# Kernel tuning notes

Hardware: AMD Instinct MI355X
Metric: run time of the kernel (lower is better)

The kernel has to match this reference:

```python
import jax, jax.numpy as jnp
import numpy as np

EPS = 1e-6
H, KV, HD, FF = 16, 8, 128, 3072

def rmsnorm(x, scale):
    # qwen3_compatible: compute in fp32, scale, cast back
    xf = x.astype(jnp.float32)
    var = jnp.mean(xf * xf, axis=-1, keepdims=True)
    return ((xf * jax.lax.rsqrt(var + EPS)) * scale).astype(x.dtype)

def apply_rope(x, cos, sin):
    # x: [b, h, s, d]; cos/sin: [s, d]
    d = x.shape[-1]
    x1, x2 = x[..., : d // 2], x[..., d // 2 :]
    rotated = jnp.concatenate([-x2, x1], axis=-1)
    return (x * cos[None, None] + rotated * sin[None, None]).astype(x.dtype)

def setup_inputs() -> dict:
    key = jax.random.key(0)
    B, S, D = 2, 2048, 1024
    ks = jax.random.split(key, 8)
    x = jax.random.normal(ks[0], (B, S, D), jnp.float32)
    mask = jnp.triu(jnp.ones((S, S), dtype=bool), k=1)  # True = masked (causal)
    # Qwen3 RoPE, base 1e6, full-dim cos/sin (halves duplicated)
    pos = jnp.arange(S, dtype=jnp.float32)
    inv_freq = 1.0 / (1e6 ** (jnp.arange(0, HD, 2, dtype=jnp.float32) / HD))
    ang = pos[:, None] * inv_freq[None, :]
    cos = jnp.concatenate([jnp.cos(ang), jnp.cos(ang)], axis=-1)
    sin = jnp.concatenate([jnp.sin(ang), jnp.sin(ang)], axis=-1)
    s = 0.02
    wq = jax.random.normal(ks[1], (D, H * HD), jnp.float32) * s
    wk = jax.random.normal(ks[2], (D, KV * HD), jnp.float32) * s
    wv = jax.random.normal(ks[3], (D, KV * HD), jnp.float32) * s
    wo = jax.random.normal(ks[4], (H * HD, D), jnp.float32) * s
    fc1 = jax.random.normal(ks[5], (D, FF), jnp.float32) * s
    fc2 = jax.random.normal(ks[6], (D, FF), jnp.float32) * s
    fc3 = jax.random.normal(ks[7], (FF, D), jnp.float32) * s
    return dict(x=x, mask=mask, cos=cos, sin=sin, wq=wq, wk=wk, wv=wv, wo=wo,
                fc1=fc1, fc2=fc2, fc3=fc3,
                norm1_scale=jnp.ones((D,), jnp.float32),
                norm2_scale=jnp.ones((D,), jnp.float32),
                q_norm_scale=jnp.ones((HD,), jnp.float32),
                k_norm_scale=jnp.ones((HD,), jnp.float32))

def reference(x, mask, cos, sin, wq, wk, wv, wo, fc1, fc2, fc3,
              norm1_scale, norm2_scale, q_norm_scale, k_norm_scale):
    B, S, D = x.shape
    G = H // KV  # GQA group size
    # --- attention sublayer ---
    h = rmsnorm(x, norm1_scale)
    q = (h @ wq).reshape(B, S, H, HD).transpose(0, 2, 1, 3)   # [b,h,s,d]
    k = (h @ wk).reshape(B, S, KV, HD).transpose(0, 2, 1, 3)  # [b,kv,s,d]
    v = (h @ wv).reshape(B, S, KV, HD).transpose(0, 2, 1, 3)
    q = rmsnorm(q, q_norm_scale)
    k = rmsnorm(k, k_norm_scale)
    q = apply_rope(q, cos, sin)
    k = apply_rope(k, cos, sin)
    k = jnp.repeat(k, G, axis=1)  # repeat_interleave over head dim
    v = jnp.repeat(v, G, axis=1)
    scores = jnp.einsum('bhqd,bhkd->bhqk', q, k)
    scores = jnp.where(mask[None, None], -jnp.inf, scores)
    w = jax.nn.softmax(scores / np.float32(np.sqrt(HD)), axis=-1)
    ctx = jnp.einsum('bhqk,bhkd->bqhd', w, v).reshape(B, S, H * HD)
    x = x + ctx @ wo
    # --- SwiGLU FFN sublayer ---
    h2 = rmsnorm(x, norm2_scale)
    ff = (jax.nn.silu(h2 @ fc1) * (h2 @ fc2)) @ fc3
    return x + ff
```

## Files before the change

### kernel.cpp

```cpp
#include <hip/hip_runtime.h>

#define B_  2
#define S_  2048
#define D_  1024
#define H_  16
#define KV_ 8
#define HD_ 128
#define FF_ 3072
#define KVB 32

typedef short bf16x8 __attribute__((ext_vector_type(8)));
typedef short bf16x4 __attribute__((ext_vector_type(4)));
typedef float f32x4 __attribute__((ext_vector_type(4)));

__device__ __forceinline__ float bf2f(unsigned short u) {
    union { float f; unsigned int i; } c; c.i = ((unsigned int)u) << 16; return c.f;
}
__device__ __forceinline__ unsigned short f2bf(float f) {
    union { float f; unsigned int i; } c; c.f = f;
    unsigned int r = c.i + 0x7fffu + ((c.i >> 16) & 1u);
    return (unsigned short)(r >> 16);
}

__device__ __forceinline__ void gload_lds16(const unsigned short* g, char* ldsbase) {
    __builtin_amdgcn_global_load_lds(
        (const __attribute__((address_space(1))) unsigned int*)g,
        (__attribute__((address_space(3))) unsigned int*)ldsbase, 16, 0, 0);
}

__device__ __forceinline__ f32x4 pv_mfma(bf16x4 a, bf16x4 b, f32x4 c) {
#if __has_builtin(__builtin_amdgcn_mfma_f32_16x16x16bf16_1k)
    return __builtin_amdgcn_mfma_f32_16x16x16bf16_1k(a, b, c, 0, 0, 0);
#elif __has_builtin(__builtin_amdgcn_mfma_f32_16x16x16_bf16)
    return __builtin_amdgcn_mfma_f32_16x16x16_bf16(a, b, c, 0, 0, 0);
#else
    f32x4 d;
    asm("v_mfma_f32_16x16x16_bf16 %0, %1, %2, %3" : "=v"(d) : "v"(a), "v"(b), "v"(c));
    return d;
#endif
}

__global__ __launch_bounds__(256)
void rmsnorm_kernel(const float* __restrict__ in, const float* __restrict__ scale,
                    unsigned short* __restrict__ out) {
    const int row = blockIdx.x;
    const int t = threadIdx.x;
    const float4 v = *reinterpret_cast<const float4*>(in + (size_t)row * D_ + t * 4);
    float s = v.x * v.x + v.y * v.y + v.z * v.z + v.w * v.w;
    #pragma unroll
    for (int o = 32; o; o >>= 1) s += __shfl_down(s, o);
    __shared__ float red[4];
    const int lane = t & 63, wid = t >> 6;
    if (lane == 0) red[wid] = s;
    __syncthreads();
    s = red[0] + red[1] + red[2] + red[3];
    const float rn = rsqrtf(s * (1.0f / D_) + 1e-6f);
    const float4 sc = *reinterpret_cast<const float4*>(scale + t * 4);
    unsigned short o4[4];
    o4[0] = f2bf(v.x * rn * sc.x);
    o4[1] = f2bf(v.y * rn * sc.y);
    o4[2] = f2bf(v.z * rn * sc.z);
    o4[3] = f2bf(v.w * rn * sc.w);
    *reinterpret_cast<ushort4*>(out + (size_t)row * D_ + t * 4) =
        *reinterpret_cast<ushort4*>(o4);
}

__global__ __launch_bounds__(256)
void wtrans_kernel(const float* __restrict__ W, unsigned short* __restrict__ Wt,
                   int K, int N) {
    __shared__ float tile[32][33];
    const int t = threadIdx.x;
    const int kt = blockIdx.x * 32, nt = blockIdx.y * 32;
    {
        const int r = t >> 3, c4 = (t & 7) * 4;
        const float4 v = *reinterpret_cast<const float4*>(W + (size_t)(kt + r) * N + nt + c4);
        tile[r][c4] = v.x; tile[r][c4 + 1] = v.y; tile[r][c4 + 2] = v.z; tile[r][c4 + 3] = v.w;
    }
    __syncthreads();
    {
        const int n = t >> 3, k4 = (t & 7) * 4;
        unsigned short o[4];
        #pragma unroll
        for (int i = 0; i < 4; i++) o[i] = f2bf(tile[k4 + i][n]);
        *reinterpret_cast<ushort4*>(Wt + (size_t)(nt + n) * K + kt + k4) =
            *reinterpret_cast<ushort4*>(o);
    }
}

template<int EPI>
__global__ __launch_bounds__(256)
void gemm_bt(const unsigned short* __restrict__ A, const unsigned short* __restrict__ Bt,
             void* __restrict__ Cout, const float* __restrict__ resid,
             int M, int N, int K) {
    constexpr int SMB = (EPI == 2) ? 34816 : 16384;
    __shared__ __align__(16) char sm[SMB];
    const int t = threadIdx.x;
    const int lane = t & 63, w = t >> 6;
    const int m0 = blockIdx.x * 128, n0 = blockIdx.y * 128;
    const int wr = w >> 1, wc = w & 1;
    const int lm = lane & 15, lg = lane >> 4;

    f32x4 acc[4][4];
    #pragma unroll
    for (int i = 0; i < 4; i++)
        #pragma unroll
        for (int j = 0; j < 4; j++) acc[i][j] = (f32x4){0.f, 0.f, 0.f, 0.f};

    const int row0 = t >> 2, kseg = (t & 3) * 8;
    const unsigned short* Ab = A + (size_t)(m0 + row0) * K + kseg;
    const unsigned short* Bb = Bt + (size_t)(n0 + row0) * K + kseg;
    const size_t rstep = (size_t)64 * K;
    char* ldsA = sm + w * 1024;
    char* ldsB = sm + 8192 + w * 1024;

    for (int k0 = 0; k0 < K; k0 += 32) {
        gload_lds16(Ab + k0, ldsA);
        gload_lds16(Ab + rstep + k0, ldsA + 4096);
        gload_lds16(Bb + k0, ldsB);
        gload_lds16(Bb + rstep + k0, ldsB + 4096);
        __syncthreads();
        bf16x8 aF[4], bF[4];
        #pragma unroll
        for (int i = 0; i < 4; i++)
            aF[i] = *reinterpret_cast<const bf16x8*>(sm + (wr * 64 + i * 16 + lm) * 64 + lg * 16);
        #pragma unroll
        for (int j = 0; j < 4; j++)
            bF[j] = *reinterpret_cast<const bf16x8*>(sm + 8192 + (wc * 64 + j * 16 + lm) * 64 + lg * 16);
        #pragma unroll
        for (int i = 0; i < 4; i++)
            #pragma unroll
            for (int j = 0; j < 4; j++)
                acc[i][j] = __builtin_amdgcn_mfma_f32_16x16x32_bf16(aF[i], bF[j], acc[i][j], 0, 0, 0);
        __syncthreads();
    }

    if (EPI == 2) {
        unsigned short (*Ct)[136] = reinterpret_cast<unsigned short(*)[136]>(sm);
        #pragma unroll
        for (int i = 0; i < 4; i++)
            #pragma unroll
            for (int j = 0; j < 4; j++)
                #pragma unroll
                for (int r = 0; r < 4; r++)
                    Ct[wc * 64 + j * 16 + lm][wr * 64 + i * 16 + lg * 4 + r] = f2bf(acc[i][j][r]);
        __syncthreads();
        const int colr = t >> 1, seg = t & 1;
        unsigned short* dst = reinterpret_cast<unsigned short*>(Cout) +
                              (size_t)(n0 + colr) * M + m0 + seg * 64;
        const unsigned short* srcp = &Ct[colr][seg * 64];
        #pragma unroll
        for (int i = 0; i < 8; i++)
            reinterpret_cast<uint4*>(dst)[i] = reinterpret_cast<const uint4*>(srcp)[i];
        return;
    }

    #pragma unroll
    for (int i = 0; i < 4; i++) {
        #pragma unroll
        for (int j = 0; j < 4; j++) {
            #pragma unroll
            for (int r = 0; r < 4; r++) {
                const int row = m0 + wr * 64 + i * 16 + lg * 4 + r;
                const int col = n0 + wc * 64 + j * 16 + lm;
                const size_t idx = (size_t)row * N + col;
                if (EPI == 0) {
                    reinterpret_cast<unsigned short*>(Cout)[idx] = f2bf(acc[i][j][r]);
                } else {
                    reinterpret_cast<float*>(Cout)[idx] = resid[idx] + acc[i][j][r];
                }
            }
        }
    }
}

__global__ __launch_bounds__(128)
void qknorm_rope_kernel(unsigned short* __restrict__ qk, const float* __restrict__ scale,
                        const float* __restrict__ cosb, const float* __restrict__ sinb,
                        int nheads) {
    const int row = blockIdx.x;
    const int head = blockIdx.y;
    const int s = row & (S_ - 1);
    const int t = threadIdx.x;
    unsigned short* p = qk + ((size_t)row * nheads + head) * HD_;
    const float v = bf2f(p[t]);
    float ss = v * v;
    #pragma unroll
    for (int o = 32; o; o >>= 1) ss += __shfl_down(ss, o);
    __shared__ float red[2];
    __shared__ float vals[HD_];
    const int lane = t & 63, wid = t >> 6;
    if (lane == 0) red[wid] = ss;
    __syncthreads();
    ss = red[0] + red[1];
    const float rn = rsqrtf(ss * (1.0f / HD_) + 1e-6f);
    const float nv = v * rn * scale[t];
    vals[t] = nv;
    __syncthreads();
    const float rot = (t < 64) ? -vals[t + 64] : vals[t - 64];
    const float c = cosb[(size_t)s * HD_ + t];
    const float sn = sinb[(size_t)s * HD_ + t];
    p[t] = f2bf(nv * c + rot * sn);
}

__global__ __launch_bounds__(256)
void fattn_kernel(const unsigned short* __restrict__ qg,
                  const unsigned short* __restrict__ kg,
                  const unsigned short* __restrict__ vtg,
                  unsigned short* __restrict__ out) {
    __shared__ __align__(16) char klds[2 * 8192];
    __shared__ __align__(16) char vtlds[2 * 9216];
    const int t = threadIdx.x;
    const int lane = t & 63, w = t >> 6;
    const int lm = lane & 15, lg = lane >> 4;
    const int g = blockIdx.x;
    const int h = g & 15, b = g >> 4;
    const int qt = (int)gridDim.y - 1 - (int)blockIdx.y;
    const int kvh = h >> 1;
    const int q0b = qt * 64;
    const int q0w = q0b + w * 16;
    const float CS = 0.12752409731504826f;

    const unsigned short* qbase = qg + ((size_t)(b * S_ + q0w + lm) * H_ + h) * HD_;
    bf16x8 qf[4];
    #pragma unroll
    for (int kk = 0; kk < 4; ++kk)
        qf[kk] = *reinterpret_cast<const bf16x8*>(qbase + kk * 32 + lg * 8);

    f32x4 acc[8];
    #pragma unroll
    for (int i = 0; i < 8; ++i) acc[i] = (f32x4){0.f, 0.f, 0.f, 0.f};
    float m = -3e38f, l = 0.f;

    const int nt = 2 * qt + 2;
    const int skv = t >> 3, sd8 = t & 7;
    const int vd = t >> 1, vseg = t & 1;
    const unsigned short* kgb = kg + ((size_t)b * S_ * KV_ + kvh) * HD_;
    const unsigned short* vgb = vtg + (size_t)(kvh * HD_) * (B_ * S_) + (size_t)b * S_;

    uint4 kr0, kr1, vr0, vr1;
    auto LOADR = [&](int kt) {
        const int kv0 = kt * KVB;
        const unsigned short* ksrc = kgb + (size_t)(kv0 + skv) * (KV_ * HD_) + sd8 * 16;
        kr0 = *reinterpret_cast<const uint4*>(ksrc);
        kr1 = *reinterpret_cast<const uint4*>(ksrc + 8);
        const unsigned short* vsrc = vgb + (size_t)vd * (B_ * S_) + kv0 + vseg * 16;
        vr0 = *reinterpret_cast<const uint4*>(vsrc);
        vr1 = *reinterpret_cast<const uint4*>(vsrc + 8);
    };
    auto WRITELDS = [&](int bufi) {
        char* kd = klds + bufi * 8192 + skv * 256;
        const int sw = (skv & 7) << 4;
        *reinterpret_cast<uint4*>(kd + ((sd8 * 32) ^ sw)) = kr0;
        *reinterpret_cast<uint4*>(kd + ((sd8 * 32 + 16) ^ sw)) = kr1;
        char* vdst = vtlds + bufi * 9216 + vd * 72 + vseg * 32;
        *reinterpret_cast<uint2*>(vdst)      = make_uint2(vr0.x, vr0.y);
        *reinterpret_cast<uint2*>(vdst + 8)  = make_uint2(vr0.z, vr0.w);
        *reinterpret_cast<uint2*>(vdst + 16) = make_uint2(vr1.x, vr1.y);
        *reinterpret_cast<uint2*>(vdst + 24) = make_uint2(vr1.z, vr1.w);
    };

    LOADR(0);
    WRITELDS(0);
    __syncthreads();

    for (int kt = 0; kt < nt; ++kt) {
        const int kv0 = kt * KVB;
        const int bufi = kt & 1;
        const bool havenext = (kt + 1 < nt);
        if (havenext) LOADR(kt + 1);
        if (kv0 <= q0w + 15) {
            f32x4 st[2];
            st[0] = (f32x4){0.f, 0.f, 0.f, 0.f};
            st[1] = (f32x4){0.f, 0.f, 0.f, 0.f};
            #pragma unroll
            for (int sub = 0; sub < 2; ++sub) {
                const int kvl = sub * 16 + lm;
                const char* krow = klds + bufi * 8192 + kvl * 256;
                const int sw = (kvl & 7) << 4;
                #pragma unroll
                for (int kk = 0; kk < 4; ++kk) {
                    const bf16x8 kf = *reinterpret_cast<const bf16x8*>(krow + ((kk * 64 + lg * 16) ^ sw));
                    st[sub] = __builtin_amdgcn_mfma_f32_16x16x32_bf16(kf, qf[kk], st[sub], 0, 0, 0);
                }
            }
            if (kv0 + KVB - 1 > q0w) {
                const int qa = q0w + lm;
                #pragma unroll
                for (int sub = 0; sub < 2; ++sub)
                    #pragma unroll
                    for (int r = 0; r < 4; ++r)
                        if (kv0 + sub * 16 + lg * 4 + r > qa) st[sub][r] = -3e38f;
            }
            float pmax = st[0][0];
            #pragma unroll
            for (int r = 1; r < 4; ++r) pmax = fmaxf(pmax, st[0][r]);
            #pragma unroll
            for (int r = 0; r < 4; ++r) pmax = fmaxf(pmax, st[1][r]);
            pmax = fmaxf(pmax, __shfl_xor(pmax, 16));
            pmax = fmaxf(pmax, __shfl_xor(pmax, 32));
            if (__any(pmax - m > 8.0f)) {
                const float mn = fmaxf(pmax, m);
                const float corr = exp2f((m - mn) * CS);
                l *= corr;
                #pragma unroll
                for (int i = 0; i < 8; ++i) acc[i] *= corr;
                m = mn;
            }
            float ps = 0.f;
            bf16x4 pb[2];
            #pragma unroll
            for (int sub = 0; sub < 2; ++sub)
                #pragma unroll
                for (int r = 0; r < 4; ++r) {
                    const float pv = exp2f((st[sub][r] - m) * CS);
                    ps += pv;
                    pb[sub][r] = (short)f2bf(pv);
                }
            ps += __shfl_xor(ps, 16);
            ps += __shfl_xor(ps, 32);
            l += ps;
            #pragma unroll
            for (int sub = 0; sub < 2; ++sub) {
                const char* vb2 = vtlds + bufi * 9216 + sub * 32 + lg * 8;
                #pragma unroll
                for (int db = 0; db < 8; ++db) {
                    const bf16x4 vf = *reinterpret_cast<const bf16x4*>(vb2 + (db * 16 + lm) * 72);
                    acc[db] = pv_mfma(vf, pb[sub], acc[db]);
                }
            }
        }
        if (havenext) WRITELDS((kt + 1) & 1);
        __syncthreads();
    }
    const float inv = 1.0f / l;
    unsigned short* ob = out + ((size_t)(b * S_ + q0w + lm) * H_ + h) * HD_ + lg * 4;
    #pragma unroll
    for (int db = 0; db < 8; ++db) {
        unsigned short r4[4];
        #pragma unroll
        for (int r = 0; r < 4; ++r) r4[r] = f2bf(acc[db][r] * inv);
        *reinterpret_cast<uint2*>(ob + db * 16) = *reinterpret_cast<uint2*>(r4);
    }
}

__global__ __launch_bounds__(256)
void silu_mul_kernel(unsigned short* __restrict__ g1, const unsigned short* __restrict__ g2, int n4) {
    const int i = blockIdx.x * 256 + threadIdx.x;
    if (i >= n4) return;
    const uint2 a = reinterpret_cast<const uint2*>(g1)[i];
    const uint2 bv = reinterpret_cast<const uint2*>(g2)[i];
    const unsigned int au[2] = {a.x, a.y}, bu[2] = {bv.x, bv.y};
    unsigned int r[2];
    #pragma unroll
    for (int j = 0; j < 2; j++) {
        const float a0 = bf2f((unsigned short)(au[j] & 0xffff));
        const float a1 = bf2f((unsigned short)(au[j] >> 16));
        const float b0 = bf2f((unsigned short)(bu[j] & 0xffff));
        const float b1 = bf2f((unsigned short)(bu[j] >> 16));
        const float s0 = a0 / (1.f + __expf(-a0)) * b0;
        const float s1 = a1 / (1.f + __expf(-a1)) * b1;
        r[j] = ((unsigned int)f2bf(s1) << 16) | (unsigned int)f2bf(s0);
    }
    reinterpret_cast<uint2*>(g1)[i] = make_uint2(r[0], r[1]);
}

extern "C" void kernel_launch(void* const* d_in, const int* in_sizes, int n_in,
                              void* d_out, int out_size, void* d_ws, size_t ws_size,
                              hipStream_t stream) {
    const float* x    = (const float*)d_in[0];
    const float* cosb = (const float*)d_in[2];
    const float* sinb = (const float*)d_in[3];
    const float* wq   = (const float*)d_in[4];
    const float* wk   = (const float*)d_in[5];
    const float* wv   = (const float*)d_in[6];
    const float* wo   = (const float*)d_in[7];
    const float* fc1  = (const float*)d_in[8];
    const float* fc2  = (const float*)d_in[9];
    const float* fc3  = (const float*)d_in[10];
    const float* n1s  = (const float*)d_in[11];
    const float* n2s  = (const float*)d_in[12];
    const float* qns  = (const float*)d_in[13];
    const float* kns  = (const float*)d_in[14];

    char* ws = (char*)d_ws;
    const int M = B_ * S_;
    float* outf = (float*)d_out;

    unsigned short* h   = (unsigned short*)(ws);
    unsigned short* qb  = (unsigned short*)(ws + 8388608);
    unsigned short* kb  = (unsigned short*)(ws + 25165824);
    unsigned short* vtb = (unsigned short*)(ws + 33554432);
    unsigned short* g1  = (unsigned short*)(ws + 8388608);
    unsigned short* g2  = (unsigned short*)(ws + 33554432);
    float*          x2  = (float*)(ws + 58720256);
    unsigned short* wqt = (unsigned short*)(ws + 75497472);
    unsigned short* wkt = (unsigned short*)(ws + 79691776);
    unsigned short* wvt = (unsigned short*)(ws + 81788928);
    unsigned short* wot = (unsigned short*)(ws + 83886080);
    unsigned short* f1t = (unsigned short*)(ws + 88080384);
    unsigned short* f2t = (unsigned short*)(ws + 94371840);
    unsigned short* f3t = (unsigned short*)(ws + 100663296);

    wtrans_kernel<<<dim3(D_ / 32, (H_ * HD_) / 32), 256, 0, stream>>>(wq, wqt, D_, H_ * HD_);
    wtrans_kernel<<<dim3(D_ / 32, (KV_ * HD_) / 32), 256, 0, stream>>>(wk, wkt, D_, KV_ * HD_);
    wtrans_kernel<<<dim3(D_ / 32, (KV_ * HD_) / 32), 256, 0, stream>>>(wv, wvt, D_, KV_ * HD_);
    wtrans_kernel<<<dim3((H_ * HD_) / 32, D_ / 32), 256, 0, stream>>>(wo, wot, H_ * HD_, D_);
    wtrans_kernel<<<dim3(D_ / 32, FF_ / 32), 256, 0, stream>>>(fc1, f1t, D_, FF_);
    wtrans_kernel<<<dim3(D_ / 32, FF_ / 32), 256, 0, stream>>>(fc2, f2t, D_, FF_);
    wtrans_kernel<<<dim3(FF_ / 32, D_ / 32), 256, 0, stream>>>(fc3, f3t, FF_, D_);

    rmsnorm_kernel<<<M, 256, 0, stream>>>(x, n1s, h);
    gemm_bt<0><<<dim3(M / 128, (H_ * HD_) / 128), 256, 0, stream>>>(h, wqt, qb, nullptr, M, H_ * HD_, D_);
    gemm_bt<0><<<dim3(M / 128, (KV_ * HD_) / 128), 256, 0, stream>>>(h, wkt, kb, nullptr, M, KV_ * HD_, D_);
    gemm_bt<2><<<dim3(M / 128, (KV_ * HD_) / 128), 256, 0, stream>>>(h, wvt, vtb, nullptr, M, KV_ * HD_, D_);
    qknorm_rope_kernel<<<dim3(M, H_), 128, 0, stream>>>(qb, qns, cosb, sinb, H_);
    qknorm_rope_kernel<<<dim3(M, KV_), 128, 0, stream>>>(kb, kns, cosb, sinb, KV_);
    fattn_kernel<<<dim3(H_ * B_, S_ / 64), 256, 0, stream>>>(qb, kb, vtb, qb);
    gemm_bt<1><<<dim3(M / 128, D_ / 128), 256, 0, stream>>>(qb, wot, x2, x, M, D_, H_ * HD_);
    rmsnorm_kernel<<<M, 256, 0, stream>>>(x2, n2s, h);
    gemm_bt<0><<<dim3(M / 128, FF_ / 128), 256, 0, stream>>>(h, f1t, g1, nullptr, M, FF_, D_);
    gemm_bt<0><<<dim3(M / 128, FF_ / 128), 256, 0, stream>>>(h, f2t, g2, nullptr, M, FF_, D_);
    silu_mul_kernel<<<(M * FF_ / 4 + 255) / 256, 256, 0, stream>>>(g1, g2, M * FF_ / 4);
    gemm_bt<1><<<dim3(M / 128, D_ / 128), 256, 0, stream>>>(g1, f3t, outf, x2, M, D_, FF_);
}
```

Before: 451.1 us.

## Fuse Q/K and FC1/FC2 projections into wide 256x256-tile GEMMs

Adds a 512-thread GEMM kernel with 256x256 tiles, double-buffered LDS staging and a workgroup swizzle. It concatenates the Q and K weights, and the FC1 and FC2 weights, so each pair runs as one wider GEMM. Downstream kernels take row strides to read the interleaved output in place, and silu_mul reads both halves from the shared buffer. This cuts launches and re-reads of the normalized activations and raises MFMA reuse per tile, but uses 128KB of LDS and more registers per block, which may limit occupancy.

Measured after the change: 423.9 us. 6.0% less time.

```diff
diff --git a/kernel.cpp b/kernel.cpp
--- a/kernel.cpp
+++ b/kernel.cpp
@@ -87,11 +87,105 @@
     }
 }
 
+__global__ __launch_bounds__(512, 2)
+void gemm256(const unsigned short* __restrict__ A, const unsigned short* __restrict__ Bt,
+             unsigned short* __restrict__ C, int M, int N, int K, int nm) {
+    __shared__ __align__(16) char lds[131072];
+    const int tid = threadIdx.x;
+    const int lane = tid & 63, w = tid >> 6;
+    const int lm = lane & 15, lg = lane >> 4;
+    const int wr = w >> 2, wc = w & 3;
+    const int nwg = gridDim.x;
+    const int cpx = nwg >> 3;
+    const int bid = blockIdx.x;
+    const int swz = (bid & 7) * cpx + (bid >> 3);
+    const int m0 = (swz % nm) * 256;
+    const int n0 = (swz / nm) * 256;
+
+    f32x4 acc[8][4];
+    #pragma unroll
+    for (int i = 0; i < 8; ++i)
+        #pragma unroll
+        for (int j = 0; j < 4; ++j) acc[i][j] = (f32x4){0.f, 0.f, 0.f, 0.f};
+
+    const int srow = tid >> 3;
+    const int skel = ((tid & 7) * 8) ^ (((tid >> 5) & 1) << 4);
+    const int flip = ((lm >> 2) & 1) << 5;
+    const int abase = (wr * 128 + lm) * 128 + ((lg * 16) ^ flip);
+    const int bbase = (wc * 64 + lm) * 128 + ((lg * 16) ^ flip);
+
+    auto stage = [&](int kt, int d) {
+        const unsigned short* ga = A + (size_t)(m0 + srow) * K + kt * 64 + skel;
+        const unsigned short* gb = Bt + (size_t)(n0 + srow) * K + kt * 64 + skel;
+        char* la = lds + d * 65536 + (w << 10);
+        char* lb = la + 32768;
+        #pragma unroll
+        for (int c = 0; c < 4; ++c) {
+            gload_lds16(ga + (size_t)(c * 64) * K, la + c * 8192);
+            gload_lds16(gb + (size_t)(c * 64) * K, lb + c * 8192);
+        }
+    };
+
+    stage(0, 0);
+    __syncthreads();
+
+    const int ntile = K >> 6;
+    for (int kt = 0; kt < ntile; ++kt) {
+        const int d = kt & 1;
+        if (kt + 1 < ntile) stage(kt + 1, d ^ 1);
+        const char* Ar = lds + d * 65536;
+        const char* Br = Ar + 32768;
+        bf16x8 bb[4][2];
+        #pragma unroll
+        for (int nf = 0; nf < 4; ++nf)
+            #pragma unroll
+            for (int s = 0; s < 2; ++s)
+                bb[nf][s] = *reinterpret_cast<const bf16x8*>(Br + bbase + nf * 2048 + s * 64);
+        bf16x8 aH[4][2];
+        #pragma unroll
+        for (int f = 0; f < 4; ++f)
+            #pragma unroll
+            for (int s = 0; s < 2; ++s)
+                aH[f][s] = *reinterpret_cast<const bf16x8*>(Ar + abase + f * 2048 + s * 64);
+        #pragma unroll
+        for (int f = 0; f < 4; ++f)
+            #pragma unroll
+            for (int nf = 0; nf < 4; ++nf)
+                #pragma unroll
+                for (int s = 0; s < 2; ++s)
+                    acc[f][nf] = __builtin_amdgcn_mfma_f32_16x16x32_bf16(
+                        aH[f][s], bb[nf][s], acc[f][nf], 0, 0, 0);
+        #pragma unroll
+        for (int f = 0; f < 4; ++f)
+            #pragma unroll
+            for (int s = 0; s < 2; ++s)
+                aH[f][s] = *reinterpret_cast<const bf16x8*>(Ar + abase + 8192 + f * 2048 + s * 64);
+        #pragma unroll
+        for (int f = 0; f < 4; ++f)
+            #pragma unroll
+            for (int nf = 0; nf < 4; ++nf)
+                #pragma unroll
+                for (int s = 0; s < 2; ++s)
+                    acc[4 + f][nf] = __builtin_amdgcn_mfma_f32_16x16x32_bf16(
+                        aH[f][s], bb[nf][s], acc[4 + f][nf], 0, 0, 0);
+        __syncthreads();
+    }
+
+    #pragma unroll
+    for (int mf = 0; mf < 8; ++mf)
+        #pragma unroll
+        for (int nf = 0; nf < 4; ++nf)
+            #pragma unroll
+            for (int r = 0; r < 4; ++r)
+                C[(size_t)(m0 + wr * 128 + mf * 16 + lg * 4 + r) * N +
+                  (n0 + wc * 64 + nf * 16 + lm)] = f2bf(acc[mf][nf][r]);
+}
+
 template<int EPI>
 __global__ __launch_bounds__(256)
 void gemm_bt(const unsigned short* __restrict__ A, const unsigned short* __restrict__ Bt,
              void* __restrict__ Cout, const float* __restrict__ resid,
-             int M, int N, int K) {
+             int M, int N, int K, int lda) {
     constexpr int SMB = (EPI == 2) ? 34816 : 16384;
     __shared__ __align__(16) char sm[SMB];
     const int t = threadIdx.x;
@@ -107,17 +201,18 @@
         for (int j = 0; j < 4; j++) acc[i][j] = (f32x4){0.f, 0.f, 0.f, 0.f};
 
     const int row0 = t >> 2, kseg = (t & 3) * 8;
-    const unsigned short* Ab = A + (size_t)(m0 + row0) * K + kseg;
+    const unsigned short* Ab = A + (size_t)(m0 + row0) * lda + kseg;
     const unsigned short* Bb = Bt + (size_t)(n0 + row0) * K + kseg;
-    const size_t rstep = (size_t)64 * K;
+    const size_t rstepA = (size_t)64 * lda;
+    const size_t rstepB = (size_t)64 * K;
     char* ldsA = sm + w * 1024;
     char* ldsB = sm + 8192 + w * 1024;
 
     for (int k0 = 0; k0 < K; k0 += 32) {
         gload_lds16(Ab + k0, ldsA);
-        gload_lds16(Ab + rstep + k0, ldsA + 4096);
+        gload_lds16(Ab + rstepA + k0, ldsA + 4096);
         gload_lds16(Bb + k0, ldsB);
-        gload_lds16(Bb + rstep + k0, ldsB + 4096);
+        gload_lds16(Bb + rstepB + k0, ldsB + 4096);
         __syncthreads();
         bf16x8 aF[4], bF[4];
         #pragma unroll
@@ -176,12 +271,12 @@
 __global__ __launch_bounds__(128)
 void qknorm_rope_kernel(unsigned short* __restrict__ qk, const float* __restrict__ scale,
                         const float* __restrict__ cosb, const float* __restrict__ sinb,
-                        int nheads) {
+                        int ld) {
     const int row = blockIdx.x;
     const int head = blockIdx.y;
     const int s = row & (S_ - 1);
     const int t = threadIdx.x;
-    unsigned short* p = qk + ((size_t)row * nheads + head) * HD_;
+    unsigned short* p = qk + (size_t)row * ld + head * HD_;
     const float v = bf2f(p[t]);
     float ss = v * v;
     #pragma unroll
@@ -206,7 +301,7 @@
 void fattn_kernel(const unsigned short* __restrict__ qg,
                   const unsigned short* __restrict__ kg,
                   const unsigned short* __restrict__ vtg,
-                  unsigned short* __restrict__ out) {
+                  unsigned short* __restrict__ out, int qld, int kld) {
     __shared__ __align__(16) char klds[2 * 8192];
     __shared__ __align__(16) char vtlds[2 * 9216];
     const int t = threadIdx.x;
@@ -220,7 +315,7 @@
     const int q0w = q0b + w * 16;
     const float CS = 0.12752409731504826f;
 
-    const unsigned short* qbase = qg + ((size_t)(b * S_ + q0w + lm) * H_ + h) * HD_;
+    const unsigned short* qbase = qg + (size_t)(b * S_ + q0w + lm) * qld + h * HD_;
     bf16x8 qf[4];
     #pragma unroll
     for (int kk = 0; kk < 4; ++kk)
@@ -234,13 +329,13 @@
     const int nt = 2 * qt + 2;
     const int skv = t >> 3, sd8 = t & 7;
     const int vd = t >> 1, vseg = t & 1;
-    const unsigned short* kgb = kg + ((size_t)b * S_ * KV_ + kvh) * HD_;
+    const unsigned short* kgb = kg + (size_t)b * S_ * kld + kvh * HD_;
     const unsigned short* vgb = vtg + (size_t)(kvh * HD_) * (B_ * S_) + (size_t)b * S_;
 
     uint4 kr0, kr1, vr0, vr1;
     auto LOADR = [&](int kt) {
         const int kv0 = kt * KVB;
-        const unsigned short* ksrc = kgb + (size_t)(kv0 + skv) * (KV_ * HD_) + sd8 * 16;
+        const unsigned short* ksrc = kgb + (size_t)(kv0 + skv) * kld + sd8 * 16;
         kr0 = *reinterpret_cast<const uint4*>(ksrc);
         kr1 = *reinterpret_cast<const uint4*>(ksrc + 8);
         const unsigned short* vsrc = vgb + (size_t)vd * (B_ * S_) + kv0 + vseg * 16;
@@ -333,7 +428,7 @@
         __syncthreads();
     }
     const float inv = 1.0f / l;
-    unsigned short* ob = out + ((size_t)(b * S_ + q0w + lm) * H_ + h) * HD_ + lg * 4;
+    unsigned short* ob = out + (size_t)(b * S_ + q0w + lm) * qld + h * HD_ + lg * 4;
     #pragma unroll
     for (int db = 0; db < 8; ++db) {
         unsigned short r4[4];
@@ -344,13 +439,16 @@
 }
 
 __global__ __launch_bounds__(256)
-void silu_mul_kernel(unsigned short* __restrict__ g1, const unsigned short* __restrict__ g2, int n4) {
+void silu_mul_kernel(unsigned short* __restrict__ g, int n4) {
     const int i = blockIdx.x * 256 + threadIdx.x;
     if (i >= n4) return;
-    const uint2 a = reinterpret_cast<const uint2*>(g1)[i];
-    const uint2 bv = reinterpret_cast<const uint2*>(g2)[i];
+    const int r = i / (FF_ / 4);
+    const int c = (i - r * (FF_ / 4)) * 4;
+    const size_t off = (size_t)r * (2 * FF_) + c;
+    const uint2 a = *reinterpret_cast<const uint2*>(g + off);
+    const uint2 bv = *reinterpret_cast<const uint2*>(g + off + FF_);
     const unsigned int au[2] = {a.x, a.y}, bu[2] = {bv.x, bv.y};
-    unsigned int r[2];
+    unsigned int rr[2];
     #pragma unroll
     for (int j = 0; j < 2; j++) {
         const float a0 = bf2f((unsigned short)(au[j] & 0xffff));
@@ -359,9 +457,9 @@
         const float b1 = bf2f((unsigned short)(bu[j] >> 16));
         const float s0 = a0 / (1.f + __expf(-a0)) * b0;
         const float s1 = a1 / (1.f + __expf(-a1)) * b1;
-        r[j] = ((unsigned int)f2bf(s1) << 16) | (unsigned int)f2bf(s0);
-    }
-    reinterpret_cast<uint2*>(g1)[i] = make_uint2(r[0], r[1]);
+        rr[j] = ((unsigned int)f2bf(s1) << 16) | (unsigned int)f2bf(s0);
+    }
+    *reinterpret_cast<uint2*>(g + off) = make_uint2(rr[0], rr[1]);
 }
 
 extern "C" void kernel_launch(void* const* d_in, const int* in_sizes, int n_in,
@@ -386,20 +484,20 @@
     const int M = B_ * S_;
     float* outf = (float*)d_out;
 
-    unsigned short* h   = (unsigned short*)(ws);
-    unsigned short* qb  = (unsigned short*)(ws + 8388608);
-    unsigned short* kb  = (unsigned short*)(ws + 25165824);
-    unsigned short* vtb = (unsigned short*)(ws + 33554432);
-    unsigned short* g1  = (unsigned short*)(ws + 8388608);
-    unsigned short* g2  = (unsigned short*)(ws + 33554432);
-    float*          x2  = (float*)(ws + 58720256);
-    unsigned short* wqt = (unsigned short*)(ws + 75497472);
-    unsigned short* wkt = (unsigned short*)(ws + 79691776);
-    unsigned short* wvt = (unsigned short*)(ws + 81788928);
-    unsigned short* wot = (unsigned short*)(ws + 83886080);
-    unsigned short* f1t = (unsigned short*)(ws + 88080384);
-    unsigned short* f2t = (unsigned short*)(ws + 94371840);
-    unsigned short* f3t = (unsigned short*)(ws + 100663296);
+    unsigned short* h    = (unsigned short*)(ws);
+    unsigned short* qkb  = (unsigned short*)(ws + 8388608);
+    unsigned short* vtb  = (unsigned short*)(ws + 33554432);
+    unsigned short* g12  = (unsigned short*)(ws + 8388608);
+    float*          x2   = (float*)(ws + 58720256);
+    unsigned short* wqkt = (unsigned short*)(ws + 75497472);
+    unsigned short* wvt  = (unsigned short*)(ws + 81788928);
+    unsigned short* wot  = (unsigned short*)(ws + 83886080);
+    unsigned short* f12t = (unsigned short*)(ws + 88080384);
+    unsigned short* f3t  = (unsigned short*)(ws + 100663296);
+    unsigned short* wqt = wqkt;
+    unsigned short* wkt = wqkt + (size_t)2048 * 1024;
+    unsigned short* f1t = f12t;
+    unsigned short* f2t = f12t + (size_t)3072 * 1024;
 
     wtrans_kernel<<<dim3(D_ / 32, (H_ * HD_) / 32), 256, 0, stream>>>(wq, wqt, D_, H_ * HD_);
     wtrans_kernel<<<dim3(D_ / 32, (KV_ * HD_) / 32), 256, 0, stream>>>(wk, wkt, D_, KV_ * HD_);
@@ -410,16 +508,14 @@
     wtrans_kernel<<<dim3(FF_ / 32, D_ / 32), 256, 0, stream>>>(fc3, f3t, FF_, D_);
 
     rmsnorm_kernel<<<M, 256, 0, stream>>>(x, n1s, h);
-    gemm_bt<0><<<dim3(M / 128, (H_ * HD_) / 128), 256, 0, stream>>>(h, wqt, qb, nullptr, M, H_ * HD_, D_);
-    gemm_bt<0><<<dim3(M / 128, (KV_ * HD_) / 128), 256, 0, stream>>>(h, wkt, kb, nullptr, M, KV_ * HD_, D_);
-    gemm_bt<2><<<dim3(M / 128, (KV_ * HD_) / 128), 256, 0, stream>>>(h, wvt, vtb, nullptr, M, KV_ * HD_, D_);
-    qknorm_rope_kernel<<<dim3(M, H_), 128, 0, stream>>>(qb, qns, cosb, sinb, H_);
-    qknorm_rope_kernel<<<dim3(M, KV_), 128, 0, stream>>>(kb, kns, cosb, sinb, KV_);
-    fattn_kernel<<<dim3(H_ * B_, S_ / 64), 256, 0, stream>>>(qb, kb, vtb, qb);
-    gemm_bt<1><<<dim3(M / 128, D_ / 128), 256, 0, stream>>>(qb, wot, x2, x, M, D_, H_ * HD_);
+    gemm256<<<(M / 256) * (3072 / 256), 512, 0, stream>>>(h, wqkt, qkb, M, 3072, D_, M / 256);
+    gemm_bt<2><<<dim3(M / 128, (KV_ * HD_) / 128), 256, 0, stream>>>(h, wvt, vtb, nullptr, M, KV_ * HD_, D_, D_);
+    qknorm_rope_kernel<<<dim3(M, H_), 128, 0, stream>>>(qkb, qns, cosb, sinb, 3072);
+    qknorm_rope_kernel<<<dim3(M, KV_), 128, 0, stream>>>(qkb + 2048, kns, cosb, sinb, 3072);
+    fattn_kernel<<<dim3(H_ * B_, S_ / 64), 256, 0, stream>>>(qkb, qkb + 2048, vtb, qkb, 3072, 3072);
+    gemm_bt<1><<<dim3(M / 128, D_ / 128), 256, 0, stream>>>(qkb, wot, x2, x, M, D_, H_ * HD_, 3072);
     rmsnorm_kernel<<<M, 256, 0, stream>>>(x2, n2s, h);
-    gemm_bt<0><<<dim3(M / 128, FF_ / 128), 256, 0, stream>>>(h, f1t, g1, nullptr, M, FF_, D_);
-    gemm_bt<0><<<dim3(M / 128, FF_ / 128), 256, 0, stream>>>(h, f2t, g2, nullptr, M, FF_, D_);
-    silu_mul_kernel<<<(M * FF_ / 4 + 255) / 256, 256, 0, stream>>>(g1, g2, M * FF_ / 4);
-    gemm_bt<1><<<dim3(M / 128, D_ / 128), 256, 0, stream>>>(g1, f3t, outf, x2, M, D_, FF_);
-}
+    gemm256<<<(M / 256) * (6144 / 256), 512, 0, stream>>>(h, f12t, g12, M, 6144, D_, M / 256);
+    silu_mul_kernel<<<(M * FF_ / 4 + 255) / 256, 256, 0, stream>>>(g12, M * FF_ / 4);
+    gemm_bt<1><<<dim3(M / 128, D_ / 128), 256, 0, stream>>>(g12, f3t, outf, x2, M, D_, FF_, 2 * FF_);
+}
```
